# Optimization experiments

Hardware: AMD Instinct MI355X
Metric: run time of the kernel (lower is better)

## Reference

```python
import jax, jax.numpy as jnp
import numpy as np

DIM = 128
HEADS = 8
WS = 4  # window_size = size/11 = 44/11
HID = DIM * 4  # ffn_expansion_factor=4


def layernorm_cl(x, w, b):
    # WithBias LayerNorm over channel dim; x: (b,c,h,w)
    x3 = x.transpose(0, 2, 3, 1)  # b,h,w,c
    mu = x3.mean(-1, keepdims=True)
    var = ((x3 - mu) ** 2).mean(-1, keepdims=True)
    y = (x3 - mu) / jnp.sqrt(var + 1e-5) * w + b
    return y.transpose(0, 3, 1, 2)


def win_part(t, ws):
    # (b,c,h,w) -> (b*nh*nw, ws*ws, c), matching torch view/permute/contiguous
    b, c, h, w = t.shape
    t = t.reshape(b, c, h // ws, ws, w // ws, ws)
    t = t.transpose(0, 2, 4, 3, 5, 1)
    return t.reshape(b * (h // ws) * (w // ws), ws * ws, c)


def conv1x1(x, w):
    # w: (Cout, Cin, 1, 1)
    return jnp.einsum('bchw,oc->bohw', x, w[:, :, 0, 0])


def dwconv3(x, w):
    # depthwise 3x3, padding 1; w: (C,1,3,3)
    return jax.lax.conv_general_dilated(
        x, w, window_strides=(1, 1), padding=[(1, 1), (1, 1)],
        dimension_numbers=('NCHW', 'OIHW', 'NCHW'),
        feature_group_count=x.shape[1])


def setup_inputs() -> dict:
    key = jax.random.key(0)
    ks = jax.random.split(key, 10)
    b, c, h, w = 4, DIM, 176, 176
    inp = {
        'x': jax.random.normal(ks[0], (b, c, h, w), jnp.float32),
        'mask': jax.random.uniform(ks[1], (b, 1, 44, 44), jnp.float32),
        'edge': jax.random.normal(ks[2], (b, c, 44, 44), jnp.float32),
        'ln1_w': jnp.ones((c,), jnp.float32),
        'ln1_b': jnp.zeros((c,), jnp.float32),
        'Wq': jax.random.normal(ks[3], (c, c), jnp.float32) * 0.02,
        'Wk': jax.random.normal(ks[4], (c, c), jnp.float32) * 0.02,
        'Wv': jax.random.normal(ks[5], (c, c), jnp.float32) * 0.02,
        'ln2_w': jnp.ones((c,), jnp.float32),
        'ln2_b': jnp.zeros((c,), jnp.float32),
        'w_in': jax.random.normal(ks[6], (2 * HID, c, 1, 1), jnp.float32) * 0.02,
        'w_dw': jax.random.normal(ks[7], (2 * HID, 1, 3, 3), jnp.float32) * 0.1,
        'w_out': jax.random.normal(ks[8], (c, HID, 1, 1), jnp.float32) * 0.02,
    }
    return inp


def _forward(x, mask, edge, ln1_w, ln1_b, Wq, Wk, Wv, ln2_w, ln2_b, w_in, w_dw, w_out):
    b, c, h, w = x.shape
    d = c // HEADS
    scale = d ** (-0.5)

    # --- attention branch ---
    xn = layernorm_cl(x, ln1_w, ln1_b)
    x0 = xn

    edge_r = jax.image.resize(edge, (b, c, h, w), method='bilinear')
    mask_r = jax.image.resize(mask, (b, mask.shape[1], h, w), method='bilinear')

    q = win_part(edge_r, WS) @ Wq.T                 # (Bw, N, c)
    x0w = win_part(x0 * mask_r, WS)
    k = x0w @ Wk.T
    v = x0w @ Wv.T

    Bw, N = q.shape[0], q.shape[1]
    q = q.reshape(Bw, N, HEADS, d)
    k = k.reshape(Bw, N, HEADS, d)
    v = v.reshape(Bw, N, HEADS, d)

    # NB: faithful to original einsum -- contracts over heads axis, giving
    # per-token d x d channel attention.
    dots = jnp.einsum('bnij,bnik->bnjk', q, k) * scale  # (Bw, N, d, d)
    attn = jax.nn.softmax(dots, axis=-1)
    out = jnp.einsum('bnjk,bnik->bnij', attn, v)        # (Bw, N, HEADS, d)
    out = out.reshape(Bw, N, c)

    # faithful (non-inverse) window merge: view -> permute -> view
    out = out.reshape(b, h // WS, w // WS, WS * WS * c)
    out = out.transpose(0, 3, 1, 2).reshape(b, c, h, w)

    x = x + out

    # --- GDFN feedforward ---
    y = layernorm_cl(x, ln2_w, ln2_b)
    y = conv1x1(y, w_in)
    y = dwconv3(y, w_dw)
    y1, y2 = jnp.split(y, 2, axis=1)
    y = jax.nn.gelu(y1, approximate=False) * y2
    y = conv1x1(y, w_out)
    return x + y


def reference(x, mask, edge, ln1_w, ln1_b, Wq, Wk, Wv, ln2_w, ln2_b, w_in, w_dw, w_out):
    return _forward(x, mask, edge, ln1_w, ln1_b, Wq, Wk, Wv, ln2_w, ln2_b, w_in, w_dw, w_out)
```

## Files before the change

kernel.cpp:

```cpp
#include <hip/hip_runtime.h>
#include <hip/hip_bf16.h>
#include <math.h>

typedef __hip_bfloat16 bf16;
typedef short bf16x8 __attribute__((ext_vector_type(8)));
typedef short bf16x4 __attribute__((ext_vector_type(4)));
typedef float floatx4 __attribute__((ext_vector_type(4)));

#define YX 30976
#define NPOS (4*YX)

__device__ __forceinline__ float ldin(const void* p, size_t i, int bf) {
  return bf ? __bfloat162float(((const bf16*)p)[i]) : ((const float*)p)[i];
}

__device__ __forceinline__ void unpack8(bf16x8 v, float* f) {
  const unsigned* u = (const unsigned*)&v;
#pragma unroll
  for (int i = 0; i < 4; ++i) {
    f[2 * i]     = __uint_as_float(u[i] << 16);
    f[2 * i + 1] = __uint_as_float(u[i] & 0xffff0000u);
  }
}

__device__ __forceinline__ void glds16(const void* g, void* l) {
  __builtin_amdgcn_global_load_lds(
      (const __attribute__((address_space(1))) unsigned int*)g,
      (__attribute__((address_space(3))) unsigned int*)l, 16, 0, 0);
}

__device__ __forceinline__ void tap44(int o, int& i0, int& i1, float& f) {
  int t = o >> 2, r = o & 3;
  int base = (r < 2) ? (t - 1) : t;
  f = (r == 0) ? 0.625f : (r == 1) ? 0.875f : (r == 2) ? 0.125f : 0.375f;
  i0 = base < 0 ? 0 : base;
  i1 = (base + 1 > 43) ? 43 : base + 1;
}

__global__ void k_sniff(const unsigned* __restrict__ ln1w, int* __restrict__ flag) {
  if (threadIdx.x == 0 && blockIdx.x == 0)
    *flag = (*ln1w == 0x3F800000u) ? 0 : 1;
}

__global__ void __launch_bounds__(256) k_castw(
    const void* __restrict__ src, bf16* __restrict__ dst, int n,
    const int* __restrict__ flag) {
  int i = blockIdx.x * 256 + threadIdx.x;
  if (i >= n) return;
  int bf = *flag;
  dst[i] = bf ? ((const bf16*)src)[i]
              : __float2bfloat16(((const float*)src)[i]);
}

__global__ void __launch_bounds__(256) k_castdw(
    const void* __restrict__ src, bf16* __restrict__ dst,
    const int* __restrict__ flag) {
  int i = blockIdx.x * 256 + threadIdx.x;
  if (i >= 9216) return;
  int bf = *flag;
  int ch = i & 511, tap = (i >> 9) % 9, g = i / (512 * 9);
  float v = ldin(src, (size_t)(g * 512 + ch) * 9 + tap, bf);
  dst[(g * 9 + tap) * 512 + ch] = __float2bfloat16(v);
}

__global__ void __launch_bounds__(256) k_ln1(
    const void* __restrict__ xin, const void* __restrict__ mask,
    const void* __restrict__ ln1w, const void* __restrict__ ln1b,
    const int* __restrict__ flag,
    bf16* __restrict__ xm_buf, bf16* __restrict__ x_pm) {
  __shared__ float sP[4][128], ssP[4][128];
  __shared__ float smu[128], srstd[128], smv[128];
  __shared__ float slw[128], slb[128];
  int bf = *flag;
  int tid = threadIdx.x;
  int p0 = blockIdx.x * 128;
  int b = p0 / YX, yx0 = p0 % YX;
  if (tid < 128) { slw[tid] = ldin(ln1w, tid, bf); slb[tid] = ldin(ln1b, tid, bf); }
  int pp = tid & 63, cq = tid >> 6;

  float v0[32], v1[32];
  float s0 = 0.f, ss0 = 0.f, s1 = 0.f, ss1 = 0.f;
  {
    size_t base = ((size_t)(b * 128 + cq * 32)) * YX + yx0 + pp * 2;
    if (bf) {
#pragma unroll
      for (int j = 0; j < 32; ++j) {
        unsigned u = *(const unsigned*)((const bf16*)xin + base + (size_t)j * YX);
        float a = __uint_as_float(u << 16);
        float c = __uint_as_float(u & 0xffff0000u);
        v0[j] = a; v1[j] = c; s0 += a; ss0 += a * a; s1 += c; ss1 += c * c;
      }
    } else {
#pragma unroll
      for (int j = 0; j < 32; ++j) {
        float2 f = *(const float2*)((const float*)xin + base + (size_t)j * YX);
        v0[j] = f.x; v1[j] = f.y; s0 += f.x; ss0 += f.x * f.x; s1 += f.y; ss1 += f.y * f.y;
      }
    }
  }
  sP[cq][pp * 2] = s0;  sP[cq][pp * 2 + 1] = s1;
  ssP[cq][pp * 2] = ss0; ssP[cq][pp * 2 + 1] = ss1;
  __syncthreads();

  if (tid < 128) {
    float st  = sP[0][tid] + sP[1][tid] + sP[2][tid] + sP[3][tid];
    float sst = ssP[0][tid] + ssP[1][tid] + ssP[2][tid] + ssP[3][tid];
    float mu = st * (1.f / 128.f);
    float var = sst * (1.f / 128.f) - mu * mu;
    smu[tid] = mu;
    srstd[tid] = rsqrtf(fmaxf(var, 0.f) + 1e-5f);
    int gyx = yx0 + tid, y = gyx / 176, x = gyx % 176;
    int y0, y1, x0, x1; float fy, fx;
    tap44(y, y0, y1, fy); tap44(x, x0, x1, fx);
    size_t mb = (size_t)b * 1936;
    float m00 = ldin(mask, mb + y0 * 44 + x0, bf);
    float m01 = ldin(mask, mb + y0 * 44 + x1, bf);
    float m10 = ldin(mask, mb + y1 * 44 + x0, bf);
    float m11 = ldin(mask, mb + y1 * 44 + x1, bf);
    smv[tid] = (m00 * (1.f - fx) + m01 * fx) * (1.f - fy) +
               (m10 * (1.f - fx) + m11 * fx) * fy;
  }
  __syncthreads();

#define WRITE_PX(K, VV)                                                        \
  {                                                                            \
    int px = pp * 2 + K;                                                       \
    float mu = smu[px], rstd = srstd[px], mv = smv[px];                        \
    size_t ob = (size_t)(p0 + px) * 128 + cq * 32;                             \
    _Pragma("unroll")                                                          \
    for (int j8 = 0; j8 < 4; ++j8) {                                           \
      bf16x8 xr, xmr;                                                          \
      _Pragma("unroll")                                                        \
      for (int i = 0; i < 8; ++i) {                                            \
        int j = j8 * 8 + i;                                                    \
        float v = VV[j];                                                       \
        int c = cq * 32 + j;                                                   \
        ((bf16*)&xr)[i]  = __float2bfloat16(v);                                \
        ((bf16*)&xmr)[i] = __float2bfloat16(((v - mu) * rstd * slw[c] + slb[c]) * mv); \
      }                                                                        \
      *(bf16x8*)(x_pm + ob + j8 * 8)   = xr;                                   \
      *(bf16x8*)(xm_buf + ob + j8 * 8) = xmr;                                  \
    }                                                                          \
  }
  WRITE_PX(0, v0)
  WRITE_PX(1, v1)
#undef WRITE_PX
}

__global__ void __launch_bounds__(256) k_edge(
    const void* __restrict__ edge, const int* __restrict__ flag,
    bf16* __restrict__ e_buf) {
  __shared__ __align__(16) float sE[2 * 44 * 128];
  int bf = *flag;
  int tid = threadIdx.x;
  int b = blockIdx.x / 176, y = blockIdx.x % 176;
  int y0, y1; float fy; tap44(y, y0, y1, fy);
  float fy0 = 1.f - fy;

#pragma unroll
  for (int r = 0; r < 2; ++r) {
    int yr = r ? y1 : y0;
#pragma unroll
    for (int it = 0; it < 6; ++it) {
      int idx = it * 256 + tid;
      if (idx < 1408) {
        int c = idx / 11, f4 = (idx % 11) * 4;
        size_t src = (size_t)(b * 128 + c) * 1936 + yr * 44 + f4;
        float4 v;
        if (bf) {
          bf16x4 bv = *(const bf16x4*)((const bf16*)edge + src);
          v.x = __bfloat162float(((bf16*)&bv)[0]);
          v.y = __bfloat162float(((bf16*)&bv)[1]);
          v.z = __bfloat162float(((bf16*)&bv)[2]);
          v.w = __bfloat162float(((bf16*)&bv)[3]);
        } else {
          v = *(const float4*)((const float*)edge + src);
        }
        float* d = sE + r * 5632 + f4 * 128 + c;
        d[0] = v.x; d[128] = v.y; d[256] = v.z; d[384] = v.w;
      }
    }
  }
  __syncthreads();

  const floatx4* sE4 = (const floatx4*)sE;
  size_t rowbase = ((size_t)b * YX + (size_t)y * 176) * 128;
#pragma unroll
  for (int it = 0; it < 11; ++it) {
    int chunk = it * 256 + tid;
    int x = chunk >> 4, c8 = (chunk & 15) * 8;
    int x0, x1; float fx; tap44(x, x0, x1, fx);
    float fx0 = 1.f - fx;
    float w00 = fy0 * fx0, w01 = fy0 * fx, w10 = fy * fx0, w11 = fy * fx;
    int c4 = c8 >> 2;
    floatx4 a0 = sE4[(0 * 44 + x0) * 32 + c4], a1 = sE4[(0 * 44 + x0) * 32 + c4 + 1];
    floatx4 b0 = sE4[(0 * 44 + x1) * 32 + c4], b1 = sE4[(0 * 44 + x1) * 32 + c4 + 1];
    floatx4 c0 = sE4[(44 + x0) * 32 + c4],     c1 = sE4[(44 + x0) * 32 + c4 + 1];
    floatx4 d0 = sE4[(44 + x1) * 32 + c4],     d1 = sE4[(44 + x1) * 32 + c4 + 1];
    bf16x8 o;
#pragma unroll
    for (int i = 0; i < 4; ++i) {
      ((bf16*)&o)[i]     = __float2bfloat16(w00 * a0[i] + w01 * b0[i] + w10 * c0[i] + w11 * d0[i]);
      ((bf16*)&o)[i + 4] = __float2bfloat16(w00 * a1[i] + w01 * b1[i] + w10 * c1[i] + w11 * d1[i]);
    }
    *(bf16x8*)(e_buf + rowbase + (size_t)x * 128 + c8) = o;
  }
}

__global__ void __launch_bounds__(384, 3) k_qkvattn(
    const bf16* __restrict__ E, const bf16* __restrict__ XM,
    const bf16* __restrict__ Wq, const bf16* __restrict__ Wk,
    const bf16* __restrict__ Wv, bf16* __restrict__ O) {
  __shared__ __align__(16) bf16 smem[32768];
  int tid = threadIdx.x;
  int wave = tid / 64, lane = tid & 63;
  int mat = wave >> 1, h = wave & 1;
  int l15 = lane & 15, quad = lane >> 4;
  int m0b = blockIdx.x * 64;

  const bf16* gA = (mat == 0) ? E : XM;
  const bf16* gW = (mat == 0) ? Wq : (mat == 1) ? Wk : Wv;

  floatx4 acc[4][4] = {};

#define STAGE(bb, kt)                                                          \
  {                                                                            \
    _Pragma("unroll")                                                          \
    for (int c = 0; c < 4; ++c)                                                \
      glds16(gW + (size_t)(h * 64 + c * 16 + l15) * 128 + (kt) + quad * 8,     \
             smem + (bb) + 4096 + mat * 4096 + (h * 4 + c) * 512);             \
    if (mat == 0) {                                                            \
      _Pragma("unroll")                                                        \
      for (int g = 0; g < 2; ++g) {                                            \
        int mm = h * 2 + g;                                                    \
        glds16(gA + (size_t)(m0b + mm * 16 + l15) * 128 + (kt) + quad * 8,     \
               smem + (bb) + mm * 512);                                        \
      }                                                                        \
    } else {                                                                   \
      int mm = wave - 2;                                                       \
      glds16(gA + (size_t)(m0b + mm * 16 + l15) * 128 + (kt) + quad * 8,       \
             smem + (bb) + 2048 + mm * 512);                                   \
    }                                                                          \
  }

  STAGE(0, 0);
  __syncthreads();

  int cur = 0;
  for (int t = 0; t < 4; ++t) {
    int nb = cur ^ 16384;
    if (t < 3) STAGE(nb, (t + 1) * 32);
    const bf16* sA = smem + cur + (mat ? 2048 : 0);
    const bf16* sW = smem + cur + 4096 + mat * 4096;
    bf16x8 af[4], bfr[4];
#pragma unroll
    for (int m = 0; m < 4; ++m)
      af[m] = *(const bf16x8*)(sA + m * 512 + lane * 8);
#pragma unroll
    for (int n = 0; n < 4; ++n)
      bfr[n] = *(const bf16x8*)(sW + (h * 4 + n) * 512 + lane * 8);
#pragma unroll
    for (int m = 0; m < 4; ++m)
#pragma unroll
      for (int n = 0; n < 4; ++n)
        acc[m][n] = __builtin_amdgcn_mfma_f32_16x16x32_bf16(bfr[n], af[m], acc[m][n], 0, 0, 0);
    __syncthreads();
    cur = nb;
  }
#undef STAGE

  if (mat < 2) {
    bf16* sT = smem + mat * 8192;
    int key = l15 & 7;
#pragma unroll
    for (int m = 0; m < 4; ++m) {
      int tokl = m * 16 + l15;
#pragma unroll
      for (int r = 0; r < 4; ++r) {
        int cidx = quad * 4 + r;
        bf16x4 o;
#pragma unroll
        for (int n = 0; n < 4; ++n) ((bf16*)&o)[n] = __float2bfloat16(acc[m][n][r]);
        *(bf16x4*)(sT + tokl * 128 + ((cidx ^ key) * 8) + h * 4) = o;
      }
    }
  } else {
    float* sVf = (float*)(smem + 16384);
    int key = l15 & 7;
#pragma unroll
    for (int m = 0; m < 4; ++m) {
      int tokl = m * 16 + l15;
#pragma unroll
      for (int n = 0; n < 4; ++n) {
        int ch4 = h * 16 + n * 4 + quad;
        floatx4 o;
#pragma unroll
        for (int r = 0; r < 4; ++r) o[r] = acc[m][n][r];
        *(floatx4*)(sVf + tokl * 128 + ((ch4 ^ key) << 2)) = o;
      }
    }
  }
  __syncthreads();

  const bf16* sQt = smem;
  const bf16* sKt = smem + 8192;
  const float* sVf = (const float*)(smem + 16384);
  for (int round = 0; round < 3; ++round) {
    int item = round * 384 + tid;
    if (item < 1024) {
      int tt = item >> 4, j = item & 15;
      int key = tt & 7;
      float qv[8];
      {
        bf16x8 q8 = *(const bf16x8*)(sQt + tt * 128 + ((j ^ key) * 8));
        unpack8(q8, qv);
      }
      float s[16], mx = -1e30f;
#pragma unroll
      for (int kk = 0; kk < 16; ++kk) {
        bf16x8 k8 = *(const bf16x8*)(sKt + tt * 128 + ((kk ^ key) * 8));
        float kv[8]; unpack8(k8, kv);
        float a = 0.f;
#pragma unroll
        for (int i = 0; i < 8; ++i) a += qv[i] * kv[i];
        a *= 0.25f;
        s[kk] = a; mx = fmaxf(mx, a);
      }
      float sum = 0.f;
#pragma unroll
      for (int kk = 0; kk < 16; ++kk) { s[kk] = __expf(s[kk] - mx); sum += s[kk]; }
      float inv = 1.f / sum;
      bf16x8 ov;
#pragma unroll
      for (int i = 0; i < 8; ++i) {
        float o = 0.f;
#pragma unroll
        for (int c4 = 0; c4 < 4; ++c4) {
          int ch4 = i * 4 + c4;
          floatx4 v4 = *(const floatx4*)(sVf + tt * 128 + ((ch4 ^ key) << 2));
#pragma unroll
          for (int r = 0; r < 4; ++r) o += s[c4 * 4 + r] * v4[r];
        }
        ((bf16*)&ov)[i] = __float2bfloat16(o * inv);
      }
      *(bf16x8*)(O + (size_t)(m0b + tt) * 128 + j * 8) = ov;
    }
  }
}

__global__ void __launch_bounds__(256) k_gemm2(
    const bf16* __restrict__ A, const bf16* __restrict__ W1,
    const bf16* __restrict__ W2, bf16* __restrict__ C1,
    bf16* __restrict__ C2) {
  __shared__ __align__(16) bf16 smem[20480];
  int tid = threadIdx.x;
  int wave = tid >> 6, lane = tid & 63;
  int row = lane & 15, kq8 = (lane >> 4) * 8;
  int m0b = blockIdx.x * 64;

  int srow = lane >> 2, scol = (lane & 3) * 8;
  const bf16* gA = A + (size_t)(m0b + wave * 16 + srow) * 128 + scol;
  const bf16* Wsrc = (wave < 2) ? W1 : W2;
  const bf16* gB = Wsrc + (size_t)((wave & 1) * 64 + srow) * 128 + scol;
  bf16* lA = smem + wave * 512;
  bf16* lB = smem + 2048 + wave * 2048;

  floatx4 acc[4][4] = {};
  glds16(gA, lA);
#pragma unroll
  for (int c = 0; c < 4; ++c) glds16(gB + c * 16 * 128, lB + c * 512);
  __syncthreads();

  int cur = 0;
  for (int t = 0; t < 4; ++t) {
    int nxt = cur ^ 1;
    if (t < 3) {
      const bf16* ga = gA + (t + 1) * 32;
      const bf16* gb = gB + (t + 1) * 32;
      glds16(ga, lA + nxt * 10240);
#pragma unroll
      for (int c = 0; c < 4; ++c)
        glds16(gb + c * 16 * 128, lB + nxt * 10240 + c * 512);
    }
    const bf16* sA = smem + cur * 10240;
    const bf16* sB = sA + 2048;
    bf16x8 af[4], bfr[4];
#pragma unroll
    for (int m = 0; m < 4; ++m)
      af[m] = *(const bf16x8*)(sA + (m * 16 + row) * 32 + kq8);
#pragma unroll
    for (int n = 0; n < 4; ++n)
      bfr[n] = *(const bf16x8*)(sB + (wave * 64 + n * 16 + row) * 32 + kq8);
#pragma unroll
    for (int m = 0; m < 4; ++m)
#pragma unroll
      for (int n = 0; n < 4; ++n)
        acc[m][n] = __builtin_amdgcn_mfma_f32_16x16x32_bf16(bfr[n], af[m], acc[m][n], 0, 0, 0);
    __syncthreads();
    cur = nxt;
  }

  bf16* dst = (wave < 2) ? C1 : C2;
  int j = lane & 15, quad = lane >> 4;
#pragma unroll
  for (int m = 0; m < 4; ++m) {
    size_t pb = (size_t)(m0b + m * 16 + j) * 128 + (wave & 1) * 64 + quad * 4;
#pragma unroll
    for (int n = 0; n < 4; ++n) {
      bf16x4 o;
#pragma unroll
      for (int r = 0; r < 4; ++r) ((bf16*)&o)[r] = __float2bfloat16(acc[m][n][r]);
      *(bf16x4*)(dst + pb + n * 16) = o;
    }
  }
}

__global__ void __launch_bounds__(256) k_merge(
    const bf16* __restrict__ AO2, const bf16* __restrict__ x_pm,
    const void* __restrict__ ln2w, const void* __restrict__ ln2b,
    const int* __restrict__ flag, bf16* __restrict__ resid,
    bf16* __restrict__ yln) {
  __shared__ __align__(16) bf16 stile[64 * 128];
  __shared__ float sP[4][64], ssP[4][64];
  __shared__ float smu[64], srstd[64];
  __shared__ float slw[128], slb[128];
  int bf = *flag;
  int tid = threadIdx.x;
  int bi = blockIdx.x;
  int iw0 = bi % 11, ih = (bi / 11) % 44, b = bi / 484;
  if (tid < 128) { slw[tid] = ldin(ln2w, tid, bf); slb[tid] = ldin(ln2b, tid, bf); }

#pragma unroll
  for (int q = 0; q < 4; ++q) {
    int idx = q * 256 + tid;
    int m = idx & 15, sp = idx >> 4;
    int dy = sp >> 4, wj = (sp >> 2) & 3, dx = sp & 3;
    int ys = ih * 4 + dy, xs = iw0 * 16 + wj * 4 + dx;
    bf16x8 v = *(const bf16x8*)(AO2 + (size_t)((b * 176 + ys) * 176 + xs) * 128 + m * 8);
    int opx = m * 4 + wj, n = dy * 4 + dx;
    *(bf16x8*)&stile[opx * 128 + (n ^ (opx & 15)) * 8] = v;
  }
  __syncthreads();

  int opx = tid & 63, cq = tid >> 6;
  int t = opx >> 2, wj = opx & 3;
  size_t p = (size_t)b * YX + t * 1936 + ih * 44 + iw0 * 4 + wj;
  float vals[32], s = 0.f, ss = 0.f;
#pragma unroll
  for (int j = 0; j < 4; ++j) {
    int nchunk = cq * 4 + j;
    bf16x8 av = *(const bf16x8*)&stile[opx * 128 + (nchunk ^ (opx & 15)) * 8];
    bf16x8 xv = *(const bf16x8*)(x_pm + p * 128 + cq * 32 + j * 8);
    float af[8], xf[8];
    unpack8(av, af); unpack8(xv, xf);
#pragma unroll
    for (int i = 0; i < 8; ++i) {
      float v = af[i] + xf[i];
      vals[j * 8 + i] = v; s += v; ss += v * v;
    }
  }
  sP[cq][opx] = s; ssP[cq][opx] = ss;
  __syncthreads();
  if (tid < 64) {
    float st  = sP[0][tid] + sP[1][tid] + sP[2][tid] + sP[3][tid];
    float sst = ssP[0][tid] + ssP[1][tid] + ssP[2][tid] + ssP[3][tid];
    float mu = st * (1.f / 128.f);
    float var = sst * (1.f / 128.f) - mu * mu;
    smu[tid] = mu;
    srstd[tid] = rsqrtf(fmaxf(var, 0.f) + 1e-5f);
  }
  __syncthreads();

  {
    float mu = smu[opx], rstd = srstd[opx];
    size_t ob = p * 128 + cq * 32;
#pragma unroll
    for (int j8 = 0; j8 < 4; ++j8) {
      bf16x8 rv, yv;
#pragma unroll
      for (int i = 0; i < 8; ++i) {
        int j = j8 * 8 + i;
        float v = vals[j];
        int c = cq * 32 + j;
        ((bf16*)&rv)[i] = __float2bfloat16(v);
        ((bf16*)&yv)[i] = __float2bfloat16((v - mu) * rstd * slw[c] + slb[c]);
      }
      *(bf16x8*)(resid + ob + j8 * 8) = rv;
      *(bf16x8*)(yln + ob + j8 * 8)   = yv;
    }
  }
}

__global__ void __launch_bounds__(256) k_dwgelu(
    const bf16* __restrict__ H1, const bf16* __restrict__ H2,
    const bf16* __restrict__ Wt, int j0, bf16* __restrict__ G) {
  int tid = blockIdx.x * 256 + threadIdx.x;
  int pos = tid >> 4, c8 = (tid & 15) * 8;
  int b = pos / YX, yx = pos % YX, y = yx / 176, x = yx % 176;
  float d1[8] = {}, d2[8] = {};
#pragma unroll
  for (int dy = 0; dy < 3; ++dy) {
    int ny = y + dy - 1;
    if (ny < 0 || ny > 175) continue;
#pragma unroll
    for (int dx = 0; dx < 3; ++dx) {
      int nx = x + dx - 1;
      if (nx < 0 || nx > 175) continue;
      int tap = dy * 3 + dx;
      size_t off = (size_t)(b * YX + ny * 176 + nx) * 128 + c8;
      float h1[8], h2[8], w1[8], w2[8];
      unpack8(*(const bf16x8*)(H1 + off), h1);
      unpack8(*(const bf16x8*)(H2 + off), h2);
      unpack8(*(const bf16x8*)(Wt + tap * 512 + j0 + c8), w1);
      unpack8(*(const bf16x8*)(Wt + (9 + tap) * 512 + j0 + c8), w2);
#pragma unroll
      for (int i = 0; i < 8; ++i) {
        d1[i] += w1[i] * h1[i];
        d2[i] += w2[i] * h2[i];
      }
    }
  }
  bf16x8 outv;
#pragma unroll
  for (int i = 0; i < 8; ++i) {
    float gl = 0.5f * d1[i] * (1.f + erff(d1[i] * 0.70710678118f));
    ((bf16*)&outv)[i] = __float2bfloat16(gl * d2[i]);
  }
  *(bf16x8*)(G + (size_t)pos * 512 + j0 + c8) = outv;
}

__global__ void __launch_bounds__(256) k_gemm_final(
    const bf16* __restrict__ G, const bf16* __restrict__ W,
    const bf16* __restrict__ resid, void* __restrict__ out,
    const int* __restrict__ flag) {
  __shared__ __align__(16) bf16 smem[16384];
  int tid = threadIdx.x;
  int wave = tid >> 6, lane = tid & 63;
  int row = lane & 15, kq8 = (lane >> 4) * 8;
  int wr = wave >> 1, wc = wave & 1;
  int m0b = blockIdx.x * 128;

  int srow = lane >> 2, scol = (lane & 3) * 8;
  const bf16* gA = G + (size_t)(m0b + wave * 32 + srow) * 512 + scol;
  const bf16* gB = W + (size_t)(wave * 32 + srow) * 512 + scol;
  bf16* lA = smem + wave * 1024;
  bf16* lB = smem + 4096 + wave * 1024;

  floatx4 acc[4][4] = {};
  glds16(gA, lA);            glds16(gA + 16 * 512, lA + 512);
  glds16(gB, lB);            glds16(gB + 16 * 512, lB + 512);
  __syncthreads();

  int cur = 0;
  for (int t = 0; t < 16; ++t) {
    int nxt = cur ^ 1;
    if (t < 15) {
      const bf16* ga = gA + (t + 1) * 32;
      const bf16* gb = gB + (t + 1) * 32;
      glds16(ga, lA + nxt * 8192);            glds16(ga + 16 * 512, lA + nxt * 8192 + 512);
      glds16(gb, lB + nxt * 8192);            glds16(gb + 16 * 512, lB + nxt * 8192 + 512);
    }
    const bf16* sA = smem + cur * 8192;
    const bf16* sB = sA + 4096;
    bf16x8 af[4], bfr[4];
#pragma unroll
    for (int m = 0; m < 4; ++m)
      af[m] = *(const bf16x8*)(sA + (wr * 64 + m * 16 + row) * 32 + kq8);
#pragma unroll
    for (int n = 0; n < 4; ++n)
      bfr[n] = *(const bf16x8*)(sB + (wc * 64 + n * 16 + row) * 32 + kq8);
#pragma unroll
    for (int m = 0; m < 4; ++m)
#pragma unroll
      for (int n = 0; n < 4; ++n)
        acc[m][n] = __builtin_amdgcn_mfma_f32_16x16x32_bf16(af[m], bfr[n], acc[m][n], 0, 0, 0);
    __syncthreads();
    cur = nxt;
  }

  {
    const bf16* gR = resid + (size_t)(m0b + wave * 32 + (lane >> 4)) * 128 + (lane & 15) * 8;
    bf16* lR = smem + wave * 32 * 128;
#pragma unroll
    for (int c = 0; c < 8; ++c)
      glds16(gR + (size_t)c * 4 * 128, lR + c * 4 * 128);
  }
  __syncthreads();

  int bfo = *flag;
  int b = m0b / YX, yx0 = m0b % YX;
  int j = lane & 15, quad = lane >> 4;
#pragma unroll
  for (int n = 0; n < 4; ++n) {
    int ch = wc * 64 + n * 16 + j;
    const bf16* rsl = smem + ch;
    size_t cb = (size_t)(b * 128 + ch) * YX + yx0;
#pragma unroll
    for (int m = 0; m < 4; ++m) {
      int pos = wr * 64 + m * 16 + quad * 4;
      float v[4];
#pragma unroll
      for (int r = 0; r < 4; ++r)
        v[r] = acc[m][n][r] + __bfloat162float(rsl[(pos + r) * 128]);
      if (bfo) {
        bf16x4 o;
#pragma unroll
        for (int r = 0; r < 4; ++r) ((bf16*)&o)[r] = __float2bfloat16(v[r]);
        *(bf16x4*)((bf16*)out + cb + pos) = o;
      } else {
        floatx4 o;
#pragma unroll
        for (int r = 0; r < 4; ++r) o[r] = v[r];
        *(floatx4*)((float*)out + cb + pos) = o;
      }
    }
  }
}

extern "C" void kernel_launch(void* const* d_in, const int* in_sizes, int n_in,
                              void* d_out, int out_size, void* d_ws, size_t ws_size,
                              hipStream_t stream) {
  const void* x    = d_in[0];
  const void* mask = d_in[1];
  const void* edge = d_in[2];
  const void* ln1w = d_in[3];
  const void* ln1b = d_in[4];
  const void* Wq   = d_in[5];
  const void* Wk   = d_in[6];
  const void* Wv   = d_in[7];
  const void* ln2w = d_in[8];
  const void* ln2b = d_in[9];
  const void* w_in = d_in[10];
  const void* w_dw = d_in[11];
  const void* w_out= d_in[12];

  char* ws = (char*)d_ws;
  const size_t SEG  = 31719424;
  const size_t GSZ  = 126877696;
  bf16* G     = (bf16*)(ws);
  bf16* B0    = (bf16*)(ws);
  bf16* B1    = (bf16*)(ws + GSZ);
  bf16* H1    = (bf16*)(ws + GSZ + SEG);
  bf16* H2    = (bf16*)(ws + GSZ + 2 * SEG);
  bf16* resid = (bf16*)(ws + GSZ + 3 * SEG);
  char* wsw   = ws + GSZ + 4 * SEG;
  bf16* wq_b   = (bf16*)(wsw);
  bf16* wk_b   = (bf16*)(wsw + 32768);
  bf16* wv_b   = (bf16*)(wsw + 65536);
  bf16* win_b  = (bf16*)(wsw + 98304);
  bf16* wout_b = (bf16*)(wsw + 98304 + 262144);
  bf16* wdwt_b = (bf16*)(wsw + 98304 + 262144 + 131072);
  int* flag    = (int*)(wsw + 98304 + 262144 + 131072 + 32768);

  k_sniff<<<1, 64, 0, stream>>>((const unsigned*)ln1w, flag);
  k_castw<<<64, 256, 0, stream>>>(Wq, wq_b, 16384, flag);
  k_castw<<<64, 256, 0, stream>>>(Wk, wk_b, 16384, flag);
  k_castw<<<64, 256, 0, stream>>>(Wv, wv_b, 16384, flag);
  k_castw<<<512, 256, 0, stream>>>(w_in, win_b, 131072, flag);
  k_castw<<<256, 256, 0, stream>>>(w_out, wout_b, 65536, flag);
  k_castdw<<<36, 256, 0, stream>>>(w_dw, wdwt_b, flag);

  k_edge<<<4 * 176, 256, 0, stream>>>(edge, flag, B0);
  k_ln1<<<NPOS / 128, 256, 0, stream>>>(x, mask, ln1w, ln1b, flag,
                                        B1, H1 );
  k_qkvattn<<<NPOS / 64, 384, 0, stream>>>(B0, B1, wq_b, wk_b, wv_b, B0);
  k_merge<<<4 * 44 * 11, 256, 0, stream>>>(B0, H1 , ln2w, ln2b, flag,
                                           resid, B1);
  for (int j0 = 0; j0 < 512; j0 += 128) {
    k_gemm2<<<NPOS / 64, 256, 0, stream>>>(B1, win_b + (size_t)j0 * 128,
                                           win_b + (size_t)(512 + j0) * 128, H1, H2);
    k_dwgelu<<<NPOS * 16 / 256, 256, 0, stream>>>(H1, H2, wdwt_b, j0, G);
  }
  k_gemm_final<<<NPOS / 128, 256, 0, stream>>>(G, wout_b, resid, d_out, flag);
}
```

Before: 627.3 us.

## Compute per-token channel attention with MFMA instead of scalar FMA loops

Rewrites the per-token 16x16 channel-attention step in the fused QKV-attention kernel so that each wave runs one token at a time, using bf16 MFMA instructions for both QK^T and PV. Softmax is reduced with cross-lane shuffles and the probabilities are rearranged with ds_bpermute. V is now stored in shared memory as bf16 instead of fp32, and the 0.25 softmax scale is folded into the Wq weight cast. The aim is to replace the heavy scalar FMA and LDS traffic of the old loop, at the cost of lower precision for V and the probabilities, plus zero-padded MFMA lanes.

```diff
diff --git a/kernel.cpp b/kernel.cpp
--- a/kernel.cpp
+++ b/kernel.cpp
@@ -43,13 +43,13 @@
 }
 
 __global__ void __launch_bounds__(256) k_castw(
-    const void* __restrict__ src, bf16* __restrict__ dst, int n,
+    const void* __restrict__ src, bf16* __restrict__ dst, int n, float scale,
     const int* __restrict__ flag) {
   int i = blockIdx.x * 256 + threadIdx.x;
   if (i >= n) return;
   int bf = *flag;
-  dst[i] = bf ? ((const bf16*)src)[i]
-              : __float2bfloat16(((const float*)src)[i]);
+  float v = ldin(src, i, bf);
+  dst[i] = __float2bfloat16(v * scale);
 }
 
 __global__ void __launch_bounds__(256) k_castdw(
@@ -285,65 +285,77 @@
       }
     }
   } else {
-    float* sVf = (float*)(smem + 16384);
+    bf16* sVt = smem + 16384;
     int key = l15 & 7;
 #pragma unroll
     for (int m = 0; m < 4; ++m) {
       int tokl = m * 16 + l15;
 #pragma unroll
       for (int n = 0; n < 4; ++n) {
-        int ch4 = h * 16 + n * 4 + quad;
-        floatx4 o;
-#pragma unroll
-        for (int r = 0; r < 4; ++r) o[r] = acc[m][n][r];
-        *(floatx4*)(sVf + tokl * 128 + ((ch4 ^ key) << 2)) = o;
-      }
-    }
-  }
-  __syncthreads();
-
-  const bf16* sQt = smem;
-  const bf16* sKt = smem + 8192;
-  const float* sVf = (const float*)(smem + 16384);
-  for (int round = 0; round < 3; ++round) {
-    int item = round * 384 + tid;
-    if (item < 1024) {
-      int tt = item >> 4, j = item & 15;
+        int head = h * 4 + n;
+        int c = head * 2 + (quad >> 1);
+        bf16x4 o;
+#pragma unroll
+        for (int r = 0; r < 4; ++r) ((bf16*)&o)[r] = __float2bfloat16(acc[m][n][r]);
+        *(bf16x4*)(sVt + tokl * 128 + ((c ^ key) * 8) + (quad & 1) * 4) = o;
+      }
+    }
+  }
+  __syncthreads();
+
+  {
+    const bf16* sQt = smem;
+    const bf16* sKt = smem + 8192;
+    const bf16* sVt = smem + 16384;
+    int g = quad;
+    const bf16x8 z8 = {};
+    int pa0 = ((l15 + 32 * g) & 63) * 4;
+    int pa1 = ((l15 + 32 * g + 16) & 63) * 4;
+    bool a1live = (g == 0);
+    bool a2live = (g < 2);
+    int vchunk = (l15 * 2 + g) & 15;
+    for (int tt = wave; tt < 64; tt += 6) {
       int key = tt & 7;
-      float qv[8];
-      {
-        bf16x8 q8 = *(const bf16x8*)(sQt + tt * 128 + ((j ^ key) * 8));
-        unpack8(q8, qv);
-      }
-      float s[16], mx = -1e30f;
-#pragma unroll
-      for (int kk = 0; kk < 16; ++kk) {
-        bf16x8 k8 = *(const bf16x8*)(sKt + tt * 128 + ((kk ^ key) * 8));
-        float kv[8]; unpack8(k8, kv);
-        float a = 0.f;
-#pragma unroll
-        for (int i = 0; i < 8; ++i) a += qv[i] * kv[i];
-        a *= 0.25f;
-        s[kk] = a; mx = fmaxf(mx, a);
-      }
-      float sum = 0.f;
-#pragma unroll
-      for (int kk = 0; kk < 16; ++kk) { s[kk] = __expf(s[kk] - mx); sum += s[kk]; }
-      float inv = 1.f / sum;
-      bf16x8 ov;
-#pragma unroll
-      for (int i = 0; i < 8; ++i) {
-        float o = 0.f;
-#pragma unroll
-        for (int c4 = 0; c4 < 4; ++c4) {
-          int ch4 = i * 4 + c4;
-          floatx4 v4 = *(const floatx4*)(sVf + tt * 128 + ((ch4 ^ key) << 2));
-#pragma unroll
-          for (int r = 0; r < 4; ++r) o += s[c4 * 4 + r] * v4[r];
-        }
-        ((bf16*)&ov)[i] = __float2bfloat16(o * inv);
-      }
-      *(bf16x8*)(O + (size_t)(m0b + tt) * 128 + j * 8) = ov;
+      const bf16* rowQ = sQt + tt * 128;
+      const bf16* rowK = sKt + tt * 128;
+      const bf16* rowV = sVt + tt * 128;
+      bf16x8 ka = *(const bf16x8*)(rowK + ((l15 ^ key) * 8));
+      bf16x8 qa = *(const bf16x8*)(rowQ + ((l15 ^ key) * 8));
+      ka = a1live ? ka : z8;
+      floatx4 c1 = {};
+      c1 = __builtin_amdgcn_mfma_f32_16x16x32_bf16(ka, qa, c1, 0, 0, 0);
+      float mx = fmaxf(fmaxf(c1[0], c1[1]), fmaxf(c1[2], c1[3]));
+      mx = fmaxf(mx, __shfl_xor(mx, 16, 64));
+      mx = fmaxf(mx, __shfl_xor(mx, 32, 64));
+      float e0 = __expf(c1[0] - mx), e1 = __expf(c1[1] - mx);
+      float e2 = __expf(c1[2] - mx), e3 = __expf(c1[3] - mx);
+      float sm = (e0 + e1) + (e2 + e3);
+      sm += __shfl_xor(sm, 16, 64);
+      sm += __shfl_xor(sm, 32, 64);
+      float inv = 1.f / sm;
+      bf16x4 pq;
+      ((bf16*)&pq)[0] = __float2bfloat16(e0 * inv);
+      ((bf16*)&pq)[1] = __float2bfloat16(e1 * inv);
+      ((bf16*)&pq)[2] = __float2bfloat16(e2 * inv);
+      ((bf16*)&pq)[3] = __float2bfloat16(e3 * inv);
+      int pk0 = ((const int*)&pq)[0], pk1 = ((const int*)&pq)[1];
+      int r0 = __builtin_amdgcn_ds_bpermute(pa0, pk0);
+      int r1 = __builtin_amdgcn_ds_bpermute(pa0, pk1);
+      int r2 = __builtin_amdgcn_ds_bpermute(pa1, pk0);
+      int r3 = __builtin_amdgcn_ds_bpermute(pa1, pk1);
+      bf16x8 pfrag;
+      ((int*)&pfrag)[0] = r0; ((int*)&pfrag)[1] = r1;
+      ((int*)&pfrag)[2] = r2; ((int*)&pfrag)[3] = r3;
+      pfrag = a2live ? pfrag : z8;
+      bf16x8 vfrag = *(const bf16x8*)(rowV + ((vchunk ^ key) * 8));
+      floatx4 c2 = {};
+      c2 = __builtin_amdgcn_mfma_f32_16x16x32_bf16(vfrag, pfrag, c2, 0, 0, 0);
+      if (a2live) {
+        bf16x4 o;
+#pragma unroll
+        for (int r = 0; r < 4; ++r) ((bf16*)&o)[r] = __float2bfloat16(c2[r]);
+        *(bf16x4*)(O + (size_t)(m0b + tt) * 128 + l15 * 8 + g * 4) = o;
+      }
     }
   }
 }
@@ -653,11 +665,11 @@
   int* flag    = (int*)(wsw + 98304 + 262144 + 131072 + 32768);
 
   k_sniff<<<1, 64, 0, stream>>>((const unsigned*)ln1w, flag);
-  k_castw<<<64, 256, 0, stream>>>(Wq, wq_b, 16384, flag);
-  k_castw<<<64, 256, 0, stream>>>(Wk, wk_b, 16384, flag);
-  k_castw<<<64, 256, 0, stream>>>(Wv, wv_b, 16384, flag);
-  k_castw<<<512, 256, 0, stream>>>(w_in, win_b, 131072, flag);
-  k_castw<<<256, 256, 0, stream>>>(w_out, wout_b, 65536, flag);
+  k_castw<<<64, 256, 0, stream>>>(Wq, wq_b, 16384, 0.25f, flag);
+  k_castw<<<64, 256, 0, stream>>>(Wk, wk_b, 16384, 1.f, flag);
+  k_castw<<<64, 256, 0, stream>>>(Wv, wv_b, 16384, 1.f, flag);
+  k_castw<<<512, 256, 0, stream>>>(w_in, win_b, 131072, 1.f, flag);
+  k_castw<<<256, 256, 0, stream>>>(w_out, wout_b, 65536, 1.f, flag);
   k_castdw<<<36, 256, 0, stream>>>(w_dw, wdwt_b, flag);
 
   k_edge<<<4 * 176, 256, 0, stream>>>(edge, flag, B0);
```

After: 623.8 us. Within noise of the previous version (-0.6%).
